# Optimization experiments

Hardware: AMD Instinct MI355X
Metric: run time of the kernel (lower is better)

The kernel has to match this reference:

```python
import jax, jax.numpy as jnp
import numpy as np

DIM = 128
NUM_HEADS = 4
SPLIT_SIZE = 8
HEAD_DIM = DIM // NUM_HEADS
SCALE = HEAD_DIM ** -0.5


def setup_inputs() -> dict:
    key = jax.random.key(0)
    qkv = jax.random.normal(key, (3, 8, 4096, DIM), dtype=jnp.float32)
    return {"qkv": qkv, "H": 64, "W": 64}


def _to_windows(x, H, W, H_sp, W_sp):
    # x: [B, L, C] -> [B*nW, num_heads, H_sp*W_sp, head_dim]
    B, L, C = x.shape
    x = x.reshape(B, H // H_sp, H_sp, W // W_sp, W_sp, C)
    x = x.transpose(0, 1, 3, 2, 4, 5).reshape(-1, H_sp * W_sp, NUM_HEADS, C // NUM_HEADS)
    return x.transpose(0, 2, 1, 3)


def reference(qkv, H, W):
    # idx=0 branch: vertical strips, H_sp = H (full height), W_sp = split_size
    H_sp, W_sp = H, SPLIT_SIZE
    B, L, C = qkv.shape[1], qkv.shape[2], qkv.shape[3]
    q = _to_windows(qkv[0], H, W, H_sp, W_sp) * SCALE
    k = _to_windows(qkv[1], H, W, H_sp, W_sp)
    v = _to_windows(qkv[2], H, W, H_sp, W_sp)
    # [nW, h, S, S] with S = H_sp*W_sp
    attn = jax.nn.softmax(jnp.einsum('whqd,whkd->whqk', q, k), axis=-1)
    x = jnp.einsum('whqk,whkd->whqd', attn, v)
    # merge heads: [nW, S, C]
    x = x.transpose(0, 2, 1, 3).reshape(-1, H_sp * W_sp, C)
    # windows2img: [B, H*W, C]
    x = x.reshape(B, H // H_sp, W // W_sp, H_sp, W_sp, C)
    x = x.transpose(0, 1, 3, 2, 4, 5).reshape(B, H * W, C)
    return x
```

## Files before the change

kernel.cpp:

```cpp
#include <hip/hip_runtime.h>


typedef __attribute__((ext_vector_type(8))) short bf16x8;
typedef __attribute__((ext_vector_type(4))) float f32x4;
typedef __attribute__((ext_vector_type(4))) int   i32x4;

#define MFMA16(a, b, c) __builtin_amdgcn_mfma_f32_16x16x32_bf16(a, b, c, 0, 0, 0)

__device__ __forceinline__ unsigned rne(float f) {
    union { float f; unsigned u; } v; v.f = f;
    return v.u + 0x7fffu + ((v.u >> 16) & 1u);
}
__device__ __forceinline__ short f2b(float f) { return (short)(rne(f) >> 16); }
__device__ __forceinline__ unsigned pkhi(unsigned lo, unsigned hi) {
    return __builtin_amdgcn_perm(hi, lo, 0x07060302u);
}

__global__ __launch_bounds__(256, 4)
void lepe_attn_r7(const float* __restrict__ qkv, float* __restrict__ out)
{
    __shared__ __align__(16) short    Ks[256 * 32];
    __shared__ __align__(16) unsigned Vt32[32 * 132];
    __shared__ __align__(16) unsigned Pb[4 * 16 * 20];

    const int tid  = threadIdx.x;
    const int wave = tid >> 6;
    const int lane = tid & 63;
    const int col  = lane & 15;
    const int quad = lane >> 4;

    const int blk  = blockIdx.x;
    const int pair = blk >> 2;
    const int qsp  = blk & 3;
    const int wi   = pair >> 2;
    const int hd   = pair & 3;
    const int b    = wi >> 3;
    const int wb   = wi & 7;
    const int chead = hd * 32;

    const size_t baseQ = (size_t)b * 524288;
    const size_t baseK = baseQ + 8u * 524288;
    const size_t baseV = baseQ + 16u * 524288;

    const int q0 = qsp * 128 + wave * 32;
    const float QS   = 0.17677669529663687f * 1.4426950408889634f;
    const float MAXB = 32.0f;
    bf16x8 qf[2];
#pragma unroll
    for (int t = 0; t < 2; ++t) {
        int q  = q0 + t * 16 + col;
        int lq = (q >> 3) * 64 + wb * 8 + (q & 7);
        const float* qp = qkv + baseQ + (size_t)lq * 128 + chead + quad * 8;
        f32x4 qa = *(const f32x4*)qp;
        f32x4 qb = *(const f32x4*)(qp + 4);
        bf16x8 qs;
#pragma unroll
        for (int j = 0; j < 4; ++j) { qs[j] = f2b(qa[j] * QS); qs[j + 4] = f2b(qb[j] * QS); }
        qf[t] = qs;
    }

    f32x4 o[2][2];
    float lsum[2][4];
#pragma unroll
    for (int t = 0; t < 2; ++t) {
        o[t][0] = (f32x4)0.0f; o[t][1] = (f32x4)0.0f;
#pragma unroll
        for (int r = 0; r < 4; ++r) lsum[t][r] = 0.0f;
    }

    unsigned* Pw = Pb + wave * 320;

    for (int stage = 0; stage < 2; ++stage) {
        if (stage) __syncthreads();
        const int keybase = stage * 256;

#pragma unroll
        for (int i = 0; i < 4; ++i) {
            int chunk = i * 256 + tid;
            int row   = chunk >> 2;
            int part  = chunk & 3;
            int gk    = keybase + row;
            int lk    = (gk >> 3) * 64 + wb * 8 + (gk & 7);
            const float* kp = qkv + baseK + (size_t)lk * 128 + chead + part * 8;
            f32x4 k0 = *(const f32x4*)kp;
            f32x4 k1 = *(const f32x4*)(kp + 4);
            bf16x8 kv;
#pragma unroll
            for (int j = 0; j < 4; ++j) { kv[j] = f2b(k0[j]); kv[j + 4] = f2b(k1[j]); }
            *(bf16x8*)&Ks[row * 32 + ((part ^ ((row >> 1) & 3)) << 3)] = kv;
        }
        {
            int p    = tid >> 1;
            int half = tid & 1;
            int k0g  = keybase + 2 * p;
            int l0   = (k0g >> 3) * 64 + wb * 8 + (k0g & 7);
            const float* va = qkv + baseV + (size_t)l0 * 128 + chead + half * 16;
            const float* vb = va + 128;
            f32x4 a[4], bb[4];
#pragma unroll
            for (int j = 0; j < 4; ++j) { a[j] = *(const f32x4*)(va + 4 * j); bb[j] = *(const f32x4*)(vb + 4 * j); }
#pragma unroll
            for (int j = 0; j < 4; ++j)
#pragma unroll
                for (int e = 0; e < 4; ++e) {
                    int dim = half * 16 + j * 4 + e;
                    Vt32[dim * 132 + p] = pkhi(rne(a[j][e]), rne(bb[j][e]));
                }
        }
        __syncthreads();

        for (int kb = 0; kb < 256; kb += 32) {
            int r0 = kb + col, r1 = kb + col + 16;
            bf16x8 kf0 = *(const bf16x8*)&Ks[r0 * 32 + ((quad ^ ((r0 >> 1) & 3)) << 3)];
            bf16x8 kf1 = *(const bf16x8*)&Ks[r1 * 32 + ((quad ^ ((r1 >> 1) & 3)) << 3)];
            const short* Vts = (const short*)Vt32;
            bf16x8 vf0 = *(const bf16x8*)&Vts[col * 264 + kb + quad * 8];
            bf16x8 vf1 = *(const bf16x8*)&Vts[(col + 16) * 264 + kb + quad * 8];

#pragma unroll
            for (int t = 0; t < 2; ++t) {
                f32x4 s0 = MFMA16(qf[t], kf0, (f32x4)0.0f);
                f32x4 s1 = MFMA16(qf[t], kf1, (f32x4)0.0f);
#pragma unroll
                for (int r = 0; r < 4; ++r) {
                    float p0 = __builtin_amdgcn_exp2f(s0[r] - MAXB);
                    float p1 = __builtin_amdgcn_exp2f(s1[r] - MAXB);
                    Pw[(quad * 4 + r) * 20 + col] = pkhi(rne(p0), rne(p1));
                    lsum[t][r] += p0 + p1;
                }
                asm volatile("" ::: "memory");
                const unsigned* pr = Pw + col * 20 + ((quad & 1) << 3);
                i32x4 da = *(const i32x4*)pr;
                i32x4 db = *(const i32x4*)(pr + 4);
                unsigned sel = (quad < 2) ? 0x05040100u : 0x07060302u;
                i32x4 fr;
                fr[0] = (int)__builtin_amdgcn_perm((unsigned)da[1], (unsigned)da[0], sel);
                fr[1] = (int)__builtin_amdgcn_perm((unsigned)da[3], (unsigned)da[2], sel);
                fr[2] = (int)__builtin_amdgcn_perm((unsigned)db[1], (unsigned)db[0], sel);
                fr[3] = (int)__builtin_amdgcn_perm((unsigned)db[3], (unsigned)db[2], sel);
                bf16x8 pf = __builtin_bit_cast(bf16x8, fr);
                asm volatile("" ::: "memory");
                o[t][0] = MFMA16(pf, vf0, o[t][0]);
                o[t][1] = MFMA16(pf, vf1, o[t][1]);
            }
        }
    }

    const size_t baseO = (size_t)b * 524288;
#pragma unroll
    for (int t = 0; t < 2; ++t) {
#pragma unroll
        for (int r = 0; r < 4; ++r) {
            float s = lsum[t][r];
            s += __shfl_xor(s, 1);
            s += __shfl_xor(s, 2);
            s += __shfl_xor(s, 4);
            s += __shfl_xor(s, 8);
            float inv = 1.0f / s;
            int q  = q0 + t * 16 + quad * 4 + r;
            int lq = (q >> 3) * 64 + wb * 8 + (q & 7);
            float* orow = out + baseO + (size_t)lq * 128 + chead;
            orow[col]      = o[t][0][r] * inv;
            orow[col + 16] = o[t][1][r] * inv;
        }
    }
}

extern "C" void kernel_launch(void* const* d_in, const int* in_sizes, int n_in,
                              void* d_out, int out_size, void* d_ws, size_t ws_size,
                              hipStream_t stream) {
    const float* qkv = (const float*)d_in[0];
    float* out = (float*)d_out;
    lepe_attn_r7<<<dim3(1024), dim3(256), 0, stream>>>(qkv, out);
}
```

Before: 107.9 us.

## Compute transposed scores so P stays in registers, permute V key order

The QK^T MFMA now swaps its operands so each lane holds scores for one query column across consecutive keys. The P fragment for the PV MFMA can then be packed directly in registers, which removes the per-wave LDS staging buffer, its stores and loads, and the perm shuffles. To match the new key ordering, V is written into shared memory with a permuted slot mapping. Row sums are reduced across quads and broadcast with a shuffle at the end.

```diff
diff --git a/kernel.cpp b/kernel.cpp
--- a/kernel.cpp
+++ b/kernel.cpp
@@ -17,11 +17,10 @@
 }
 
 __global__ __launch_bounds__(256, 4)
-void lepe_attn_r7(const float* __restrict__ qkv, float* __restrict__ out)
+void lepe_attn_r10(const float* __restrict__ qkv, float* __restrict__ out)
 {
     __shared__ __align__(16) short    Ks[256 * 32];
     __shared__ __align__(16) unsigned Vt32[32 * 132];
-    __shared__ __align__(16) unsigned Pb[4 * 16 * 20];
 
     const int tid  = threadIdx.x;
     const int wave = tid >> 6;
@@ -60,15 +59,9 @@
     }
 
     f32x4 o[2][2];
-    float lsum[2][4];
+    float lsum[2] = {0.0f, 0.0f};
 #pragma unroll
-    for (int t = 0; t < 2; ++t) {
-        o[t][0] = (f32x4)0.0f; o[t][1] = (f32x4)0.0f;
-#pragma unroll
-        for (int r = 0; r < 4; ++r) lsum[t][r] = 0.0f;
-    }
-
-    unsigned* Pw = Pb + wave * 320;
+    for (int t = 0; t < 2; ++t) { o[t][0] = (f32x4)0.0f; o[t][1] = (f32x4)0.0f; }
 
     for (int stage = 0; stage < 2; ++stage) {
         if (stage) __syncthreads();
@@ -96,6 +89,8 @@
             int l0   = (k0g >> 3) * 64 + wb * 8 + (k0g & 7);
             const float* va = qkv + baseV + (size_t)l0 * 128 + chead + half * 16;
             const float* vb = va + 128;
+            int kk   = (p & 15) * 2;
+            int slot = (p >> 4) * 16 + ((kk & 12) + ((kk >> 4) & 1) * 2 + ((kk & 3) >> 1));
             f32x4 a[4], bb[4];
 #pragma unroll
             for (int j = 0; j < 4; ++j) { a[j] = *(const f32x4*)(va + 4 * j); bb[j] = *(const f32x4*)(vb + 4 * j); }
@@ -104,7 +99,7 @@
 #pragma unroll
                 for (int e = 0; e < 4; ++e) {
                     int dim = half * 16 + j * 4 + e;
-                    Vt32[dim * 132 + p] = pkhi(rne(a[j][e]), rne(bb[j][e]));
+                    Vt32[dim * 132 + slot] = pkhi(rne(a[j][e]), rne(bb[j][e]));
                 }
         }
         __syncthreads();
@@ -119,27 +114,21 @@
 
 #pragma unroll
             for (int t = 0; t < 2; ++t) {
-                f32x4 s0 = MFMA16(qf[t], kf0, (f32x4)0.0f);
-                f32x4 s1 = MFMA16(qf[t], kf1, (f32x4)0.0f);
+                f32x4 s0 = MFMA16(kf0, qf[t], (f32x4)0.0f);
+                f32x4 s1 = MFMA16(kf1, qf[t], (f32x4)0.0f);
+                float p0[4], p1[4];
 #pragma unroll
                 for (int r = 0; r < 4; ++r) {
-                    float p0 = __builtin_amdgcn_exp2f(s0[r] - MAXB);
-                    float p1 = __builtin_amdgcn_exp2f(s1[r] - MAXB);
-                    Pw[(quad * 4 + r) * 20 + col] = pkhi(rne(p0), rne(p1));
-                    lsum[t][r] += p0 + p1;
+                    p0[r] = __builtin_amdgcn_exp2f(s0[r] - MAXB);
+                    p1[r] = __builtin_amdgcn_exp2f(s1[r] - MAXB);
                 }
-                asm volatile("" ::: "memory");
-                const unsigned* pr = Pw + col * 20 + ((quad & 1) << 3);
-                i32x4 da = *(const i32x4*)pr;
-                i32x4 db = *(const i32x4*)(pr + 4);
-                unsigned sel = (quad < 2) ? 0x05040100u : 0x07060302u;
+                lsum[t] += (p0[0] + p0[1]) + (p0[2] + p0[3]) + (p1[0] + p1[1]) + (p1[2] + p1[3]);
                 i32x4 fr;
-                fr[0] = (int)__builtin_amdgcn_perm((unsigned)da[1], (unsigned)da[0], sel);
-                fr[1] = (int)__builtin_amdgcn_perm((unsigned)da[3], (unsigned)da[2], sel);
-                fr[2] = (int)__builtin_amdgcn_perm((unsigned)db[1], (unsigned)db[0], sel);
-                fr[3] = (int)__builtin_amdgcn_perm((unsigned)db[3], (unsigned)db[2], sel);
+                fr[0] = (int)pkhi(rne(p0[0]), rne(p0[1]));
+                fr[1] = (int)pkhi(rne(p0[2]), rne(p0[3]));
+                fr[2] = (int)pkhi(rne(p1[0]), rne(p1[1]));
+                fr[3] = (int)pkhi(rne(p1[2]), rne(p1[3]));
                 bf16x8 pf = __builtin_bit_cast(bf16x8, fr);
-                asm volatile("" ::: "memory");
                 o[t][0] = MFMA16(pf, vf0, o[t][0]);
                 o[t][1] = MFMA16(pf, vf1, o[t][1]);
             }
@@ -149,14 +138,12 @@
     const size_t baseO = (size_t)b * 524288;
 #pragma unroll
     for (int t = 0; t < 2; ++t) {
+        float ls = lsum[t];
+        ls += __shfl_xor(ls, 16, 64);
+        ls += __shfl_xor(ls, 32, 64);
 #pragma unroll
         for (int r = 0; r < 4; ++r) {
-            float s = lsum[t][r];
-            s += __shfl_xor(s, 1);
-            s += __shfl_xor(s, 2);
-            s += __shfl_xor(s, 4);
-            s += __shfl_xor(s, 8);
-            float inv = 1.0f / s;
+            float inv = 1.0f / __shfl(ls, quad * 4 + r, 64);
             int q  = q0 + t * 16 + quad * 4 + r;
             int lq = (q >> 3) * 64 + wb * 8 + (q & 7);
             float* orow = out + baseO + (size_t)lq * 128 + chead;
@@ -171,5 +158,5 @@
                               hipStream_t stream) {
     const float* qkv = (const float*)d_in[0];
     float* out = (float*)d_out;
-    lepe_attn_r7<<<dim3(1024), dim3(256), 0, stream>>>(qkv, out);
+    lepe_attn_r10<<<dim3(1024), dim3(256), 0, stream>>>(qkv, out);
 }
```

New measurement: 152.6 us. 1.41x slower.
